# Kernel optimization log

Measured on AMD Instinct MI355X. Metric: run time of the kernel, lower is better.

The kernel has to match this reference:

```python
import jax, jax.numpy as jnp
import numpy as np

C_IN = 32
C_OUT = 32
C_EMB = 16
GROUPS = 4
NEG_SLOPE = 0.2
EPS = 1e-5


def conv3d(x, w, b, pad):
    out = jax.lax.conv_general_dilated(
        x, w, window_strides=(1, 1, 1), padding=[(pad, pad)] * 3,
        dimension_numbers=('NCDHW', 'OIDHW', 'NCDHW'))
    return out + b[None, :, None, None, None]


def group_norm(x, gamma, beta):
    B, C = x.shape[0], x.shape[1]
    xr = x.reshape(B, GROUPS, C // GROUPS, -1)
    mu = xr.mean(axis=(2, 3), keepdims=True)
    var = xr.var(axis=(2, 3), keepdims=True)
    xr = (xr - mu) * jax.lax.rsqrt(var + EPS)
    x = xr.reshape(x.shape)
    return x * gamma[None, :, None, None, None] + beta[None, :, None, None, None]


def lrelu(x):
    return jnp.where(x >= 0, x, NEG_SLOPE * x)


def residual_block(x, w1, b1, g1, be1, w2, b2, g2, be2, ws, bs, gs, bes):
    h = lrelu(group_norm(conv3d(x, w1, b1, 1), g1, be1))
    h = group_norm(conv3d(h, w2, b2, 1), g2, be2)  # no activation on last conv
    r = group_norm(conv3d(x, ws, bs, 0), gs, bes)
    return lrelu(h + r)


def radial_field():
    # identity_grid_like(zeros(1,1,3,3,3), normalize=True) -> coords in [-1,1]
    c = jnp.array([-1.0, 0.0, 1.0], dtype=jnp.float32)
    gh, gw, gd = jnp.meshgrid(c, c, c, indexing='ij')
    # to_token: [1,3,27] -> transpose -> [27,3]
    return jnp.stack([gh, gw, gd], axis=0).reshape(3, 27).T  # [27, 3]


def extract_patches(x):
    # x: [B, C, H+2, W+2, D+2] -> K: [B, H, W, D, 27, C], unfold order (kh, kw, kd)
    B, C = x.shape[0], x.shape[1]
    H, W, D = x.shape[2] - 2, x.shape[3] - 2, x.shape[4] - 2
    slices = [x[:, :, i:i + H, j:j + W, k:k + D]
              for i in range(3) for j in range(3) for k in range(3)]
    patches = jnp.stack(slices, axis=2)  # [B, C, 27, H, W, D]
    return patches.transpose(0, 3, 4, 5, 2, 1)  # [B, H, W, D, 27, C]


def setup_inputs() -> dict:
    key = jax.random.key(0)
    ks = jax.random.split(key, 16)
    sc = 0.05
    inp = {
        'feat_moving': jax.random.normal(ks[0], (1, C_IN, 64, 64, 64), jnp.float32),
        'feat_fixed': jax.random.normal(ks[1], (1, C_IN, 64, 64, 64), jnp.float32),
        'w1': jax.random.normal(ks[2], (C_OUT, C_IN, 3, 3, 3), jnp.float32) * sc,
        'b1': jnp.zeros((C_OUT,), jnp.float32),
        'g1': jnp.ones((C_OUT,), jnp.float32),
        'be1': jnp.zeros((C_OUT,), jnp.float32),
        'w2': jax.random.normal(ks[3], (C_OUT, C_OUT, 3, 3, 3), jnp.float32) * sc,
        'b2': jnp.zeros((C_OUT,), jnp.float32),
        'g2': jnp.ones((C_OUT,), jnp.float32),
        'be2': jnp.zeros((C_OUT,), jnp.float32),
        'ws': jax.random.normal(ks[4], (C_OUT, C_IN, 1, 1, 1), jnp.float32) * sc,
        'bs': jnp.zeros((C_OUT,), jnp.float32),
        'gs': jnp.ones((C_OUT,), jnp.float32),
        'bes': jnp.zeros((C_OUT,), jnp.float32),
        'wp': jax.random.normal(ks[5], (C_EMB, C_OUT, 1, 1, 1), jnp.float32) * sc,
        'bp': jnp.zeros((C_EMB,), jnp.float32),
    }
    return inp


def reference(feat_moving, feat_fixed, w1, b1, g1, be1, w2, b2, g2, be2,
              ws, bs, gs, bes, wp, bp):
    fixed = residual_block(feat_fixed, w1, b1, g1, be1, w2, b2, g2, be2, ws, bs, gs, bes)
    moving = residual_block(feat_moving, w1, b1, g1, be1, w2, b2, g2, be2, ws, bs, gs, bes)
    fixed_emb = conv3d(fixed, wp, bp, 0)  # [B, 16, H, W, D]
    moving_pad = jnp.pad(moving, ((0, 0), (0, 0), (1, 1), (1, 1), (1, 1)), mode='edge')
    moving_emb = conv3d(moving_pad, wp, bp, 0)  # [B, 16, H+2, W+2, D+2]

    Q = fixed_emb.transpose(0, 2, 3, 4, 1)  # [B, H, W, D, 16]
    K = extract_patches(moving_emb)          # [B, H, W, D, 27, 16]
    R = radial_field()                        # [27, 3]

    temp = jnp.sqrt(jnp.float32(C_EMB))
    scores = jnp.einsum('bhwdc,bhwdpc->bhwdp', Q, K) / temp
    attn = jax.nn.softmax(scores, axis=-1)
    disp = jnp.einsum('bhwdp,pr->bhwdr', attn, R)  # [B, H, W, D, 3]
    return disp.transpose(0, 4, 1, 2, 3)  # [B, 3, H, W, D]
```

## Files before the change

### kernel.cpp

```cpp
#include <hip/hip_runtime.h>
#include <hip/hip_bf16.h>

#define NVOX (64*64*64)
#define NB32 (32*NVOX)

typedef short s8v __attribute__((ext_vector_type(8)));
typedef float f4v __attribute__((ext_vector_type(4)));

__device__ inline ushort bfb(float f) {
    __hip_bfloat16 h = __float2bfloat16(f);
    return *reinterpret_cast<ushort*>(&h);
}
__device__ inline float bf2f(ushort u) {
    unsigned x = (unsigned)u << 16;
    return __builtin_bit_cast(float, x);
}

__global__ __launch_bounds__(256) void prep_kernel(
    const float* __restrict__ w1, const float* __restrict__ w2,
    const float* __restrict__ wsw,
    ushort* __restrict__ wB1, ushort* __restrict__ wB2,
    ushort* __restrict__ wsB, float* __restrict__ stats)
{
    if (blockIdx.x == 0 && threadIdx.x < 48) stats[threadIdx.x] = 0.f;
    int i = blockIdx.x * 256 + threadIdx.x;
    if (i < 1024) wsB[i] = bfb(wsw[i]);
    if (i < 32 * 32 * 27) {
        int co  = i / 864;
        int rem = i - co * 864;
        int ci  = rem / 27;
        int tap = rem - ci * 27;
        wB1[(tap * 32 + co) * 32 + ci] = bfb(w1[i]);
        wB2[(tap * 32 + co) * 32 + ci] = bfb(w2[i]);
    }
}

__global__ __launch_bounds__(256) void tobf_skip_kernel(
    const float* __restrict__ in0, const float* __restrict__ in1,
    const ushort* __restrict__ wsB, const float* __restrict__ bsb,
    ushort* __restrict__ featB, ushort* __restrict__ skipB,
    float* __restrict__ stats)
{
    const int img = blockIdx.y;
    const float* __restrict__ in = img ? in1 : in0;
    const int t = threadIdx.x;
    const int lane = t & 63, wid = t >> 6;
    const int m = lane & 15, kc = lane >> 4;
    const int vb = blockIdx.x * 256 + wid * 64;

    ushort* __restrict__ fo = featB + (size_t)img * NVOX * 32;

    s8v bfrag[4];
#pragma unroll
    for (int nt = 0; nt < 4; ++nt) {
        const int vox = vb + nt * 16 + m;
        s8v pk;
#pragma unroll
        for (int j = 0; j < 8; ++j)
            pk[j] = (short)bfb(in[(kc * 8 + j) * NVOX + vox]);
        bfrag[nt] = pk;
        *reinterpret_cast<s8v*>(fo + (size_t)vox * 32 + kc * 8) = pk;
    }

    const s8v* __restrict__ wv = reinterpret_cast<const s8v*>(wsB);
    const s8v a0 = wv[m * 4 + kc];
    const s8v a1 = wv[(m + 16) * 4 + kc];
    f4v acc[2][4] = {};
#pragma unroll
    for (int nt = 0; nt < 4; ++nt) {
        acc[0][nt] = __builtin_amdgcn_mfma_f32_16x16x32_bf16(a0, bfrag[nt], acc[0][nt], 0, 0, 0);
        acc[1][nt] = __builtin_amdgcn_mfma_f32_16x16x32_bf16(a1, bfrag[nt], acc[1][nt], 0, 0, 0);
    }

    ushort* __restrict__ sko = skipB + (size_t)img * NVOX * 32;
    float s0 = 0.f, q0 = 0.f, s1 = 0.f, q1 = 0.f;
#pragma unroll
    for (int mt = 0; mt < 2; ++mt) {
#pragma unroll
        for (int nt = 0; nt < 4; ++nt) {
            const f4v a = acc[mt][nt];
            ushort4 pk;
            float xs[4];
#pragma unroll
            for (int j = 0; j < 4; ++j) {
                const int co = mt * 16 + kc * 4 + j;
                xs[j] = a[j] + bsb[co];
            }
            pk.x = bfb(xs[0]); pk.y = bfb(xs[1]); pk.z = bfb(xs[2]); pk.w = bfb(xs[3]);
            *reinterpret_cast<ushort4*>(
                sko + (size_t)(vb + nt * 16 + m) * 32 + mt * 16 + kc * 4) = pk;
#pragma unroll
            for (int j = 0; j < 4; ++j) {
                if (mt == 0) { s0 += xs[j]; q0 += xs[j] * xs[j]; }
                else         { s1 += xs[j]; q1 += xs[j] * xs[j]; }
            }
        }
    }

    __shared__ float red[4][8];
    float v4[4] = {s0, q0, s1, q1};
#pragma unroll
    for (int k = 0; k < 4; ++k) {
        float x = v4[k];
        x += __shfl_xor(x, 1, 64);
        x += __shfl_xor(x, 2, 64);
        x += __shfl_xor(x, 4, 64);
        x += __shfl_xor(x, 8, 64);
        x += __shfl_xor(x, 16, 64);
        v4[k] = x;
    }
    if (lane == 0)  { red[wid][0] = v4[0]; red[wid][1] = v4[1]; red[wid][4] = v4[2]; red[wid][5] = v4[3]; }
    if (lane == 32) { red[wid][2] = v4[0]; red[wid][3] = v4[1]; red[wid][6] = v4[2]; red[wid][7] = v4[3]; }
    __syncthreads();
    if (t < 8) {
        atomicAdd(&stats[img * 24 + 16 + t],
                  red[0][t] + red[1][t] + red[2][t] + red[3][t]);
    }
}

__global__ __launch_bounds__(256) void gn_transpose_kernel(
    const ushort* __restrict__ cA, const float* __restrict__ stats,
    const float* __restrict__ gamma, const float* __restrict__ beta,
    ushort* __restrict__ outB)
{
    const int img = blockIdx.y;
    const ushort* __restrict__ in = cA + (size_t)img * NB32;
    ushort* __restrict__ op = outB + (size_t)img * NVOX * 32;
    const int v = blockIdx.x * 256 + threadIdx.x;
    const float Minv = 1.f / (8.f * (float)NVOX);
    float mu[4], rs[4];
#pragma unroll
    for (int g = 0; g < 4; ++g) {
        const float s = stats[img * 24 + 2 * g], q = stats[img * 24 + 2 * g + 1];
        mu[g] = s * Minv;
        rs[g] = rsqrtf(q * Minv - mu[g] * mu[g] + 1e-5f);
    }
#pragma unroll
    for (int ciq = 0; ciq < 4; ++ciq) {
        s8v pk;
#pragma unroll
        for (int j = 0; j < 8; ++j) {
            const int c = ciq * 8 + j;
            const int g = c >> 3;
            const float sc = rs[g] * gamma[c];
            const float sh = beta[c] - mu[g] * sc;
            float y = bf2f(in[c * NVOX + v]) * sc + sh;
            y = y >= 0.f ? y : 0.2f * y;
            pk[j] = (short)bfb(y);
        }
        *reinterpret_cast<s8v*>(op + (size_t)v * 32 + ciq * 8) = pk;
    }
}

__global__ __launch_bounds__(512) void conv3_mfma_kernel(
    const ushort* __restrict__ inB,
    const ushort* __restrict__ wB, const float* __restrict__ bias,
    ushort* __restrict__ outB, float* __restrict__ stats, int layer)
{
    __shared__ __align__(16) ushort tile[4 * 1226 * 8];
    __shared__ float red[8][8];

    const int img = blockIdx.y;
    const ushort* __restrict__ src = inB + (size_t)img * NVOX * 32;
    const int bx = blockIdx.x;
    const int bd = bx & 1, bw = (bx >> 1) & 15, bh = bx >> 5;
    const int t = threadIdx.x;

    const int gd0 = bd * 32 - 1, gh0 = bh * 4 - 1, gw0 = bw * 4 - 1;
    s8v* __restrict__ tvw = reinterpret_cast<s8v*>(tile);
    for (int u = t; u < 4896; u += 512) {
        const int r   = u >> 2;
        const int ciq = u & 3;
        const int hw = r / 34, dd = r - hw * 34;
        const int hh = hw / 6, ww = hw - hh * 6;
        const int gh = gh0 + hh, gw = gw0 + ww, gd = gd0 + dd;
        s8v val = {0, 0, 0, 0, 0, 0, 0, 0};
        if (((unsigned)gh < 64u) && ((unsigned)gw < 64u) && ((unsigned)gd < 64u))
            val = *reinterpret_cast<const s8v*>(
                src + (size_t)(((gh << 12) + (gw << 6) + gd) << 5) + (ciq << 3));
        tvw[ciq * 1226 + r] = val;
    }
    __syncthreads();

    const int lane = t & 63, wid = t >> 6;
    const int m = lane & 15, kc = lane >> 4;
    const int hp = wid & 3, wh = wid >> 2;

    int pre8[2][2];
#pragma unroll
    for (int i2 = 0; i2 < 2; ++i2)
#pragma unroll
    for (int dt = 0; dt < 2; ++dt)
        pre8[i2][dt] = kc * 1226 + (hp * 6 + wh * 2 + i2) * 34 + dt * 16 + m;

    const int wlane = m * 4 + kc;
    const s8v* __restrict__ tv = reinterpret_cast<const s8v*>(tile);
    const s8v* __restrict__ wv = reinterpret_cast<const s8v*>(wB);

    f4v acc[2][2][2] = {};
#pragma unroll
    for (int tap = 0; tap < 27; ++tap) {
        const int dh = tap / 9, dw = (tap / 3) % 3, dd = tap % 3;
        const int toff = (dh * 6 + dw) * 34 + dd;
        const s8v bf0 = wv[tap * 128 + wlane];
        const s8v bf1 = wv[tap * 128 + 64 + wlane];
#pragma unroll
        for (int i2 = 0; i2 < 2; ++i2)
#pragma unroll
        for (int dt = 0; dt < 2; ++dt) {
            const s8v a = tv[pre8[i2][dt] + toff];
            acc[i2][dt][0] = __builtin_amdgcn_mfma_f32_16x16x32_bf16(a, bf0, acc[i2][dt][0], 0, 0, 0);
            acc[i2][dt][1] = __builtin_amdgcn_mfma_f32_16x16x32_bf16(a, bf1, acc[i2][dt][1], 0, 0, 0);
        }
    }

    ushort* __restrict__ outi = outB + (size_t)img * NB32;
    const float b0 = bias[m], b1 = bias[m + 16];
    ushort* __restrict__ op0 = outi + (size_t)m * NVOX;
    ushort* __restrict__ op1 = outi + (size_t)(m + 16) * NVOX;
    float gsum[2] = {0.f, 0.f}, gsq[2] = {0.f, 0.f};
#pragma unroll
    for (int i2 = 0; i2 < 2; ++i2) {
#pragma unroll
        for (int dt = 0; dt < 2; ++dt) {
            const int v = ((bh * 4 + hp) << 12) + ((bw * 4 + wh * 2 + i2) << 6)
                        + bd * 32 + dt * 16 + kc * 4;
#pragma unroll
            for (int nt = 0; nt < 2; ++nt) {
                const f4v a = acc[i2][dt][nt];
                const float bb = nt ? b1 : b0;
                const float x0 = a[0] + bb, x1 = a[1] + bb, x2 = a[2] + bb, x3 = a[3] + bb;
                ushort4 pk;
                pk.x = bfb(x0); pk.y = bfb(x1); pk.z = bfb(x2); pk.w = bfb(x3);
                *reinterpret_cast<ushort4*>((nt ? op1 : op0) + v) = pk;
                gsum[nt] += x0 + x1 + x2 + x3;
                gsq[nt]  += x0 * x0 + x1 * x1 + x2 * x2 + x3 * x3;
            }
        }
    }

#pragma unroll
    for (int nt = 0; nt < 2; ++nt) {
        float s = gsum[nt], q = gsq[nt];
        s += __shfl_xor(s, 16, 64); q += __shfl_xor(q, 16, 64);
        s += __shfl_xor(s, 32, 64); q += __shfl_xor(q, 32, 64);
        s += __shfl_xor(s, 1, 64);  q += __shfl_xor(q, 1, 64);
        s += __shfl_xor(s, 2, 64);  q += __shfl_xor(q, 2, 64);
        s += __shfl_xor(s, 4, 64);  q += __shfl_xor(q, 4, 64);
        if (lane == 0) { const int g = nt * 2;     red[wid][g * 2] = s; red[wid][g * 2 + 1] = q; }
        if (lane == 8) { const int g = nt * 2 + 1; red[wid][g * 2] = s; red[wid][g * 2 + 1] = q; }
    }
    __syncthreads();
    if (t < 8) {
        float s = 0.f;
#pragma unroll
        for (int ww8 = 0; ww8 < 8; ++ww8) s += red[ww8][t];
        atomicAdd(&stats[img * 24 + layer * 8 + t], s);
    }
}

__global__ __launch_bounds__(256) void combine_kernel(
    const ushort* __restrict__ Bb, const ushort* __restrict__ Sk,
    const float* __restrict__ stats,
    const float* __restrict__ g2, const float* __restrict__ be2,
    const float* __restrict__ gs, const float* __restrict__ bes,
    const float* __restrict__ wp, const float* __restrict__ bp,
    ushort* __restrict__ embB)
{
    const int img = blockIdx.y;
    const int v   = blockIdx.x * 256 + threadIdx.x;
    const float Minv = 1.f / (8.f * (float)NVOX);
    float mu1[4], rs1[4], mu2[4], rs2[4];
#pragma unroll
    for (int g = 0; g < 4; ++g) {
        float s = stats[img * 24 + 8 + 2 * g], q = stats[img * 24 + 8 + 2 * g + 1];
        mu1[g] = s * Minv; rs1[g] = rsqrtf(q * Minv - mu1[g] * mu1[g] + 1e-5f);
        s = stats[img * 24 + 16 + 2 * g]; q = stats[img * 24 + 16 + 2 * g + 1];
        mu2[g] = s * Minv; rs2[g] = rsqrtf(q * Minv - mu2[g] * mu2[g] + 1e-5f);
    }
    const ushort* __restrict__ bb = Bb + (size_t)img * NB32;
    const ushort* __restrict__ sk = Sk + ((size_t)img * NVOX + v) * 32;
    float o[32];
#pragma unroll
    for (int cq = 0; cq < 4; ++cq) {
        const s8v sv8 = *reinterpret_cast<const s8v*>(sk + cq * 8);
#pragma unroll
        for (int j = 0; j < 8; ++j) {
            const int c = cq * 8 + j;
            const int g = c >> 3;
            const float hv = (bf2f(bb[c * NVOX + v]) - mu1[g]) * rs1[g] * g2[c] + be2[c];
            const float sv = (bf2f((ushort)sv8[j]) - mu2[g]) * rs2[g] * gs[c] + bes[c];
            const float tv = hv + sv;
            o[c] = tv >= 0.f ? tv : 0.2f * tv;
        }
    }
    ushort* __restrict__ eo = embB + ((size_t)img * NVOX + v) * 16;
#pragma unroll
    for (int eq = 0; eq < 2; ++eq) {
        s8v pk;
#pragma unroll
        for (int j = 0; j < 8; ++j) {
            const int e = eq * 8 + j;
            float s = bp[e];
#pragma unroll
            for (int c = 0; c < 32; ++c) s += wp[e * 32 + c] * o[c];
            pk[j] = (short)bfb(s);
        }
        *reinterpret_cast<s8v*>(eo + eq * 8) = pk;
    }
}

__global__ __launch_bounds__(256) void attn_kernel(
    const ushort* __restrict__ embB, float* __restrict__ out)
{
    const int v = blockIdx.x * 256 + threadIdx.x;
    const int h = v >> 12, w = (v >> 6) & 63, d = v & 63;
    const ushort* __restrict__ Qp = embB + (size_t)v * 16;
    const ushort* __restrict__ Kp = embB + (size_t)NVOX * 16;
    float q[16];
    {
        const s8v q0 = *reinterpret_cast<const s8v*>(Qp);
        const s8v q1 = *reinterpret_cast<const s8v*>(Qp + 8);
#pragma unroll
        for (int j = 0; j < 8; ++j) { q[j] = bf2f((ushort)q0[j]); q[8 + j] = bf2f((ushort)q1[j]); }
    }
    float sc[27];
    float m = -1e30f;
#pragma unroll
    for (int ih = 0; ih < 3; ++ih)
#pragma unroll
    for (int iw = 0; iw < 3; ++iw)
#pragma unroll
    for (int id = 0; id < 3; ++id) {
        int hh = h + ih - 1; hh = hh < 0 ? 0 : (hh > 63 ? 63 : hh);
        int ww = w + iw - 1; ww = ww < 0 ? 0 : (ww > 63 ? 63 : ww);
        int dd = d + id - 1; dd = dd < 0 ? 0 : (dd > 63 ? 63 : dd);
        const ushort* __restrict__ kp = Kp + (size_t)((hh << 12) + (ww << 6) + dd) * 16;
        const s8v k0 = *reinterpret_cast<const s8v*>(kp);
        const s8v k1 = *reinterpret_cast<const s8v*>(kp + 8);
        float s = 0.f;
#pragma unroll
        for (int j = 0; j < 8; ++j)
            s += q[j] * bf2f((ushort)k0[j]) + q[8 + j] * bf2f((ushort)k1[j]);
        s *= 0.25f;
        sc[(ih * 3 + iw) * 3 + id] = s;
        m = fmaxf(m, s);
    }
    float den = 0.f;
#pragma unroll
    for (int p = 0; p < 27; ++p) { sc[p] = __expf(sc[p] - m); den += sc[p]; }
    const float inv = 1.f / den;
    float r0 = 0.f, r1 = 0.f, r2 = 0.f;
#pragma unroll
    for (int ih = 0; ih < 3; ++ih)
#pragma unroll
    for (int iw = 0; iw < 3; ++iw)
#pragma unroll
    for (int id = 0; id < 3; ++id) {
        const float a = sc[(ih * 3 + iw) * 3 + id] * inv;
        r0 += a * (float)(ih - 1);
        r1 += a * (float)(iw - 1);
        r2 += a * (float)(id - 1);
    }
    out[v]            = r0;
    out[NVOX + v]     = r1;
    out[2 * NVOX + v] = r2;
}

extern "C" void kernel_launch(void* const* d_in, const int* in_sizes, int n_in,
                              void* d_out, int out_size, void* d_ws, size_t ws_size,
                              hipStream_t stream)
{
    (void)in_sizes; (void)n_in; (void)out_size; (void)ws_size;
    const float* feat_moving = (const float*)d_in[0];
    const float* feat_fixed  = (const float*)d_in[1];
    const float* w1  = (const float*)d_in[2];
    const float* b1  = (const float*)d_in[3];
    const float* g1  = (const float*)d_in[4];
    const float* be1 = (const float*)d_in[5];
    const float* w2  = (const float*)d_in[6];
    const float* b2  = (const float*)d_in[7];
    const float* g2  = (const float*)d_in[8];
    const float* be2 = (const float*)d_in[9];
    const float* wsw = (const float*)d_in[10];
    const float* bs  = (const float*)d_in[11];
    const float* gs  = (const float*)d_in[12];
    const float* bes = (const float*)d_in[13];
    const float* wp  = (const float*)d_in[14];
    const float* bp  = (const float*)d_in[15];

    char* base = (char*)d_ws;
    ushort* featB = (ushort*)base;
    ushort* cA    = (ushort*)(base + (32ull << 20));
    ushort* AB    = (ushort*)(base + (64ull << 20));
    ushort* cB    = (ushort*)(base + (96ull << 20));
    ushort* skipB = (ushort*)(base + (128ull << 20));
    ushort* embB  = (ushort*)(base + (32ull << 20));
    float*  stats = (float*)(base + (160ull << 20));
    ushort* wB1   = (ushort*)(stats + 64);
    ushort* wB2   = wB1 + 27648;
    ushort* wsB   = wB2 + 27648;

    prep_kernel<<<108, 256, 0, stream>>>(w1, w2, wsw, wB1, wB2, wsB, stats);
    tobf_skip_kernel<<<dim3(1024, 2), 256, 0, stream>>>(feat_fixed, feat_moving, wsB, bs,
                                                        featB, skipB, stats);
    conv3_mfma_kernel<<<dim3(512, 2), 512, 0, stream>>>(featB, wB1, b1, cA, stats, 0);
    gn_transpose_kernel<<<dim3(1024, 2), 256, 0, stream>>>(cA, stats, g1, be1, AB);
    conv3_mfma_kernel<<<dim3(512, 2), 512, 0, stream>>>(AB, wB2, b2, cB, stats, 1);
    combine_kernel<<<dim3(1024, 2), 256, 0, stream>>>(cB, skipB, stats, g2, be2, gs, bes, wp, bp, embB);
    attn_kernel<<<1024, 256, 0, stream>>>(embB, (float*)d_out);
}
```

Measured before the change: 198.4 us.

## Fuse GroupNorm+LeakyReLU into conv2 tile load and store conv outputs channel-last

Removes the separate gn_transpose kernel by applying the first GroupNorm and LeakyReLU while staging the input tile of the second conv. Conv outputs are now written channel-last, voxel-major, so the next conv and the combine kernel read contiguous 8-channel vectors. The conv block shrinks to 256 threads with a 2-row h tile, doubling the grid. This saves one full read and write pass over the intermediate activation. In exchange the conv epilogue does scalar 2-byte strided stores, and the halo overhead per tile is larger.

```diff
diff --git a/kernel.cpp b/kernel.cpp
--- a/kernel.cpp
+++ b/kernel.cpp
@@ -118,47 +118,16 @@
     }
 }
 
-__global__ __launch_bounds__(256) void gn_transpose_kernel(
-    const ushort* __restrict__ cA, const float* __restrict__ stats,
-    const float* __restrict__ gamma, const float* __restrict__ beta,
-    ushort* __restrict__ outB)
-{
-    const int img = blockIdx.y;
-    const ushort* __restrict__ in = cA + (size_t)img * NB32;
-    ushort* __restrict__ op = outB + (size_t)img * NVOX * 32;
-    const int v = blockIdx.x * 256 + threadIdx.x;
-    const float Minv = 1.f / (8.f * (float)NVOX);
-    float mu[4], rs[4];
-#pragma unroll
-    for (int g = 0; g < 4; ++g) {
-        const float s = stats[img * 24 + 2 * g], q = stats[img * 24 + 2 * g + 1];
-        mu[g] = s * Minv;
-        rs[g] = rsqrtf(q * Minv - mu[g] * mu[g] + 1e-5f);
-    }
-#pragma unroll
-    for (int ciq = 0; ciq < 4; ++ciq) {
-        s8v pk;
-#pragma unroll
-        for (int j = 0; j < 8; ++j) {
-            const int c = ciq * 8 + j;
-            const int g = c >> 3;
-            const float sc = rs[g] * gamma[c];
-            const float sh = beta[c] - mu[g] * sc;
-            float y = bf2f(in[c * NVOX + v]) * sc + sh;
-            y = y >= 0.f ? y : 0.2f * y;
-            pk[j] = (short)bfb(y);
-        }
-        *reinterpret_cast<s8v*>(op + (size_t)v * 32 + ciq * 8) = pk;
-    }
-}
-
-__global__ __launch_bounds__(512) void conv3_mfma_kernel(
+__global__ __launch_bounds__(256) void conv3_mfma_kernel(
     const ushort* __restrict__ inB,
     const ushort* __restrict__ wB, const float* __restrict__ bias,
-    ushort* __restrict__ outB, float* __restrict__ stats, int layer)
-{
-    __shared__ __align__(16) ushort tile[4 * 1226 * 8];
-    __shared__ float red[8][8];
+    const float* __restrict__ gamma, const float* __restrict__ beta,
+    int apply_gn, int layer,
+    ushort* __restrict__ outB, float* __restrict__ stats)
+{
+    __shared__ __align__(16) ushort tile[4 * 818 * 8];
+    __shared__ float red[4][8];
+    __shared__ float gscs[32], gshs[32];
 
     const int img = blockIdx.y;
     const ushort* __restrict__ src = inB + (size_t)img * NVOX * 32;
@@ -166,32 +135,62 @@
     const int bd = bx & 1, bw = (bx >> 1) & 15, bh = bx >> 5;
     const int t = threadIdx.x;
 
-    const int gd0 = bd * 32 - 1, gh0 = bh * 4 - 1, gw0 = bw * 4 - 1;
+    if (t < 32) {
+        if (apply_gn) {
+            const float Minv = 1.f / (8.f * (float)NVOX);
+            const int g = t >> 3;
+            const float s = stats[img * 24 + 2 * g], q = stats[img * 24 + 2 * g + 1];
+            const float mu = s * Minv;
+            const float rs = rsqrtf(q * Minv - mu * mu + 1e-5f);
+            const float sc = rs * gamma[t];
+            gscs[t] = sc; gshs[t] = beta[t] - mu * sc;
+        } else {
+            gscs[t] = 1.f; gshs[t] = 0.f;
+        }
+    }
+    __syncthreads();
+
+    const int ciq_s = t & 3;
+    float sc8[8], sh8[8];
+#pragma unroll
+    for (int j = 0; j < 8; ++j) { sc8[j] = gscs[ciq_s * 8 + j]; sh8[j] = gshs[ciq_s * 8 + j]; }
+
+    const int gd0 = bd * 32 - 1, gh0 = bh * 2 - 1, gw0 = bw * 4 - 1;
     s8v* __restrict__ tvw = reinterpret_cast<s8v*>(tile);
-    for (int u = t; u < 4896; u += 512) {
-        const int r   = u >> 2;
-        const int ciq = u & 3;
+    for (int u = t; u < 3264; u += 256) {
+        const int r = u >> 2;
         const int hw = r / 34, dd = r - hw * 34;
         const int hh = hw / 6, ww = hw - hh * 6;
         const int gh = gh0 + hh, gw = gw0 + ww, gd = gd0 + dd;
         s8v val = {0, 0, 0, 0, 0, 0, 0, 0};
-        if (((unsigned)gh < 64u) && ((unsigned)gw < 64u) && ((unsigned)gd < 64u))
+        if (((unsigned)gh < 64u) && ((unsigned)gw < 64u) && ((unsigned)gd < 64u)) {
             val = *reinterpret_cast<const s8v*>(
-                src + (size_t)(((gh << 12) + (gw << 6) + gd) << 5) + (ciq << 3));
-        tvw[ciq * 1226 + r] = val;
+                src + (size_t)(((gh << 12) + (gw << 6) + gd) << 5) + (ciq_s << 3));
+            if (apply_gn) {
+                s8v o;
+#pragma unroll
+                for (int j = 0; j < 8; ++j) {
+                    float y = bf2f((ushort)val[j]) * sc8[j] + sh8[j];
+                    y = y >= 0.f ? y : 0.2f * y;
+                    o[j] = (short)bfb(y);
+                }
+                val = o;
+            }
+        }
+        tvw[ciq_s * 818 + r] = val;
     }
     __syncthreads();
 
     const int lane = t & 63, wid = t >> 6;
     const int m = lane & 15, kc = lane >> 4;
-    const int hp = wid & 3, wh = wid >> 2;
+    const int hp = wid & 1, wh = wid >> 1;
 
     int pre8[2][2];
 #pragma unroll
     for (int i2 = 0; i2 < 2; ++i2)
 #pragma unroll
     for (int dt = 0; dt < 2; ++dt)
-        pre8[i2][dt] = kc * 1226 + (hp * 6 + wh * 2 + i2) * 34 + dt * 16 + m;
+        pre8[i2][dt] = kc * 818 + (hp * 6 + wh * 2 + i2) * 34 + dt * 16 + m;
 
     const int wlane = m * 4 + kc;
     const s8v* __restrict__ tv = reinterpret_cast<const s8v*>(tile);
@@ -214,27 +213,27 @@
         }
     }
 
-    ushort* __restrict__ outi = outB + (size_t)img * NB32;
+    ushort* __restrict__ outi = outB + (size_t)img * NVOX * 32;
     const float b0 = bias[m], b1 = bias[m + 16];
-    ushort* __restrict__ op0 = outi + (size_t)m * NVOX;
-    ushort* __restrict__ op1 = outi + (size_t)(m + 16) * NVOX;
     float gsum[2] = {0.f, 0.f}, gsq[2] = {0.f, 0.f};
 #pragma unroll
     for (int i2 = 0; i2 < 2; ++i2) {
 #pragma unroll
         for (int dt = 0; dt < 2; ++dt) {
-            const int v = ((bh * 4 + hp) << 12) + ((bw * 4 + wh * 2 + i2) << 6)
-                        + bd * 32 + dt * 16 + kc * 4;
+            const int v0 = ((bh * 2 + hp) << 12) + ((bw * 4 + wh * 2 + i2) << 6)
+                         + bd * 32 + dt * 16 + kc * 4;
 #pragma unroll
             for (int nt = 0; nt < 2; ++nt) {
                 const f4v a = acc[i2][dt][nt];
                 const float bb = nt ? b1 : b0;
-                const float x0 = a[0] + bb, x1 = a[1] + bb, x2 = a[2] + bb, x3 = a[3] + bb;
-                ushort4 pk;
-                pk.x = bfb(x0); pk.y = bfb(x1); pk.z = bfb(x2); pk.w = bfb(x3);
-                *reinterpret_cast<ushort4*>((nt ? op1 : op0) + v) = pk;
-                gsum[nt] += x0 + x1 + x2 + x3;
-                gsq[nt]  += x0 * x0 + x1 * x1 + x2 * x2 + x3 * x3;
+                const int co = nt ? (m + 16) : m;
+#pragma unroll
+                for (int j = 0; j < 4; ++j) {
+                    const float x = a[j] + bb;
+                    outi[(size_t)(v0 + j) * 32 + co] = bfb(x);
+                    gsum[nt] += x;
+                    gsq[nt]  += x * x;
+                }
             }
         }
     }
@@ -252,10 +251,8 @@
     }
     __syncthreads();
     if (t < 8) {
-        float s = 0.f;
-#pragma unroll
-        for (int ww8 = 0; ww8 < 8; ++ww8) s += red[ww8][t];
-        atomicAdd(&stats[img * 24 + layer * 8 + t], s);
+        atomicAdd(&stats[img * 24 + layer * 8 + t],
+                  red[0][t] + red[1][t] + red[2][t] + red[3][t]);
     }
 }
 
@@ -278,17 +275,18 @@
         s = stats[img * 24 + 16 + 2 * g]; q = stats[img * 24 + 16 + 2 * g + 1];
         mu2[g] = s * Minv; rs2[g] = rsqrtf(q * Minv - mu2[g] * mu2[g] + 1e-5f);
     }
-    const ushort* __restrict__ bb = Bb + (size_t)img * NB32;
+    const ushort* __restrict__ bb = Bb + ((size_t)img * NVOX + v) * 32;
     const ushort* __restrict__ sk = Sk + ((size_t)img * NVOX + v) * 32;
     float o[32];
 #pragma unroll
     for (int cq = 0; cq < 4; ++cq) {
+        const s8v bv8 = *reinterpret_cast<const s8v*>(bb + cq * 8);
         const s8v sv8 = *reinterpret_cast<const s8v*>(sk + cq * 8);
 #pragma unroll
         for (int j = 0; j < 8; ++j) {
             const int c = cq * 8 + j;
             const int g = c >> 3;
-            const float hv = (bf2f(bb[c * NVOX + v]) - mu1[g]) * rs1[g] * g2[c] + be2[c];
+            const float hv = (bf2f((ushort)bv8[j]) - mu1[g]) * rs1[g] * g2[c] + be2[c];
             const float sv = (bf2f((ushort)sv8[j]) - mu2[g]) * rs2[g] * gs[c] + bes[c];
             const float tv = hv + sv;
             o[c] = tv >= 0.f ? tv : 0.2f * tv;
@@ -392,11 +390,10 @@
     char* base = (char*)d_ws;
     ushort* featB = (ushort*)base;
     ushort* cA    = (ushort*)(base + (32ull << 20));
-    ushort* AB    = (ushort*)(base + (64ull << 20));
-    ushort* cB    = (ushort*)(base + (96ull << 20));
-    ushort* skipB = (ushort*)(base + (128ull << 20));
-    ushort* embB  = (ushort*)(base + (32ull << 20));
-    float*  stats = (float*)(base + (160ull << 20));
+    ushort* cB    = (ushort*)(base + (64ull << 20));
+    ushort* skipB = (ushort*)(base + (96ull << 20));
+    ushort* embB  = (ushort*)base;
+    float*  stats = (float*)(base + (128ull << 20));
     ushort* wB1   = (ushort*)(stats + 64);
     ushort* wB2   = wB1 + 27648;
     ushort* wsB   = wB2 + 27648;
@@ -404,9 +401,11 @@
     prep_kernel<<<108, 256, 0, stream>>>(w1, w2, wsw, wB1, wB2, wsB, stats);
     tobf_skip_kernel<<<dim3(1024, 2), 256, 0, stream>>>(feat_fixed, feat_moving, wsB, bs,
                                                         featB, skipB, stats);
-    conv3_mfma_kernel<<<dim3(512, 2), 512, 0, stream>>>(featB, wB1, b1, cA, stats, 0);
-    gn_transpose_kernel<<<dim3(1024, 2), 256, 0, stream>>>(cA, stats, g1, be1, AB);
-    conv3_mfma_kernel<<<dim3(512, 2), 512, 0, stream>>>(AB, wB2, b2, cB, stats, 1);
-    combine_kernel<<<dim3(1024, 2), 256, 0, stream>>>(cB, skipB, stats, g2, be2, gs, bes, wp, bp, embB);
+    conv3_mfma_kernel<<<dim3(1024, 2), 256, 0, stream>>>(featB, wB1, b1, g1, be1, 0, 0,
+                                                         cA, stats);
+    conv3_mfma_kernel<<<dim3(1024, 2), 256, 0, stream>>>(cA, wB2, b2, g1, be1, 1, 1,
+                                                         cB, stats);
+    combine_kernel<<<dim3(1024, 2), 256, 0, stream>>>(cB, skipB, stats, g2, be2, gs, bes,
+                                                      wp, bp, embB);
     attn_kernel<<<1024, 256, 0, stream>>>(embB, (float*)d_out);
 }
```

After: 224.8 us. 13.3% more time.
